# Kernel tuning notes

Measured on AMD Instinct MI355X. Metric: run time of the kernel, lower is better.

Reference implementation:

```python
import jax, jax.numpy as jnp
import numpy as np

K = 4  # kNN neighbors


def build_edges(density_maps, k):
    B, _, H, W = density_maps.shape
    N = H * W
    flat = density_maps.reshape(B, N)
    # [B, N, N] pairwise absolute density distance
    dist = jnp.abs(flat[:, :, None] - flat[:, None, :])
    # k nearest (excluding self at position 0)
    tgt = jnp.argsort(dist, axis=2)[:, :, 1:k + 1]  # [B, N, k]
    src = jnp.broadcast_to(jnp.arange(N)[None, :, None], (B, N, k))
    offset = (jnp.arange(B) * N)[:, None, None]
    src = (src + offset).reshape(-1)
    tgt = (tgt + offset).reshape(-1)
    n_total = B * N
    loops = jnp.arange(n_total)
    row = jnp.concatenate([src, loops])  # source nodes
    col = jnp.concatenate([tgt, loops])  # target nodes
    return row, col, n_total


def gcn_conv(x, row, col, W, b, n_nodes):
    # symmetric deg^-1/2 normalization, deg computed on target (col)
    deg = jax.ops.segment_sum(jnp.ones_like(col, dtype=x.dtype), col, num_segments=n_nodes)
    dinv = jnp.where(deg > 0, jax.lax.rsqrt(deg), 0.0)
    norm = dinv[row] * dinv[col]  # [E]
    h = x @ W  # transform first, then propagate
    msg = norm[:, None] * h[row]
    out = jax.ops.segment_sum(msg, col, num_segments=n_nodes)
    return out + b


def setup_inputs() -> dict:
    key = jax.random.key(0)
    k1, k2, k3, k4, k5, k6 = jax.random.split(key, 6)
    B, Cin, Chid, Cout, H, W = 4, 256, 512, 256, 64, 64
    density_maps = jax.random.uniform(k1, (B, 1, H, W), dtype=jnp.float32)
    feature_maps = jax.random.normal(k2, (B, Cin, H, W), dtype=jnp.float32)
    W1 = jax.random.normal(k3, (Cin, Chid), dtype=jnp.float32) * (1.0 / np.sqrt(Cin))
    b1 = jnp.zeros((Chid,), dtype=jnp.float32)
    W2 = jax.random.normal(k4, (Chid, Cout), dtype=jnp.float32) * (1.0 / np.sqrt(Chid))
    b2 = jnp.zeros((Cout,), dtype=jnp.float32)
    return {"density_maps": density_maps, "feature_maps": feature_maps,
            "W1": W1, "b1": b1, "W2": W2, "b2": b2}


def reference(density_maps, feature_maps, W1, b1, W2, b2):
    B, Cin, H, Wd = feature_maps.shape
    row, col, n_total = build_edges(density_maps, K)
    # [B,C,H,W] -> [B*H*W, C] node features
    x = feature_maps.transpose(0, 2, 3, 1).reshape(-1, Cin)
    h = jax.nn.relu(gcn_conv(x, row, col, W1, b1, n_total))
    out = jax.nn.relu(gcn_conv(h, row, col, W2, b2, n_total))
    return out.reshape(B, H, Wd, -1).transpose(0, 3, 1, 2)
```

## Files before the change

kernel.cpp:

```cpp
#include <hip/hip_runtime.h>
#include <hip/hip_bf16.h>
#include <stdint.h>

#define N_NODES 16384
#define NPB     4096
#define NB      4
#define KNN     4
#define WIN     12
#define NBUK    4096

typedef short bf16x8 __attribute__((ext_vector_type(8)));
typedef float f32x4 __attribute__((ext_vector_type(4)));
typedef unsigned short u16x8 __attribute__((ext_vector_type(8)));

__device__ __forceinline__ unsigned short f2bf(float f) {
  unsigned u = __float_as_uint(f);
  unsigned r = (u + 0x7fff + ((u >> 16) & 1)) >> 16;
  return (unsigned short)r;
}
__device__ __forceinline__ float bf2f(unsigned short u) {
  return __uint_as_float(((unsigned)u) << 16);
}

__global__ __launch_bounds__(1024)
void bucket_kernel(const float* __restrict__ dm,
                   unsigned long long* __restrict__ skeys_g,
                   int* __restrict__ rank_g,
                   float* __restrict__ dinv_g,
                   unsigned* __restrict__ mask_g) {
  __shared__ int sHist[4096];
  __shared__ int sCur[4096];
  __shared__ unsigned long long sKeys[4096];
  __shared__ unsigned sMask[4096];
  int* part1 = (int*)sKeys;
  int* part2 = (int*)(sKeys + 512);
  const int t = threadIdx.x, b = blockIdx.x;
  const float* d = dm + b * NPB;

  unsigned long long kv[4]; int bk[4];
#pragma unroll
  for (int r = 0; r < 4; ++r) sHist[t + r * 1024] = 0;
  __syncthreads();
#pragma unroll
  for (int r = 0; r < 4; ++r) {
    int i = t + r * 1024;
    float v = d[i];
    kv[r] = (((unsigned long long)__float_as_uint(v)) << 32) | (unsigned)i;
    int k = (int)(v * (float)NBUK); if (k > NBUK - 1) k = NBUK - 1;
    bk[r] = k;
    atomicAdd(&sHist[k], 1);
  }
  __syncthreads();
  int c0 = sHist[4 * t + 0], c1 = sHist[4 * t + 1];
  int c2 = sHist[4 * t + 2], c3 = sHist[4 * t + 3];
  part1[t] = c0 + c1 + c2 + c3;
  __syncthreads();
  if (t < 64) {
    int s = 0;
#pragma unroll
    for (int k = 0; k < 16; ++k) s += part1[16 * t + k];
    part2[t] = s;
  }
  __syncthreads();
  if (t == 0) {
    int a = 0;
    for (int u = 0; u < 64; ++u) { int v = part2[u]; part2[u] = a; a += v; }
  }
  __syncthreads();
  int base = part2[t >> 4];
  for (int k = (t >> 4) * 16; k < t; ++k) base += part1[k];
  sHist[4 * t + 0] = base; sCur[4 * t + 0] = base; base += c0;
  sHist[4 * t + 1] = base; sCur[4 * t + 1] = base; base += c1;
  sHist[4 * t + 2] = base; sCur[4 * t + 2] = base; base += c2;
  sHist[4 * t + 3] = base; sCur[4 * t + 3] = base;
  __syncthreads();
#pragma unroll
  for (int r = 0; r < 4; ++r) {
    int slot = atomicAdd(&sCur[bk[r]], 1);
    sKeys[slot] = kv[r];
  }
  __syncthreads();
#pragma unroll
  for (int r = 0; r < 4; ++r) {
    int g = t + r * 1024;
    int s0 = sHist[g];
    int s1 = (g == NPB - 1) ? NPB : sHist[g + 1];
    for (int i = s0 + 1; i < s1; ++i) {
      unsigned long long x = sKeys[i];
      int j = i - 1;
      while (j >= s0 && sKeys[j] > x) { sKeys[j + 1] = sKeys[j]; --j; }
      sKeys[j + 1] = x;
    }
  }
  __syncthreads();
#pragma unroll
  for (int r = 0; r < 4; ++r) {
    int i = t + r * 1024;
    sHist[i] = 1;
    sMask[i] = 0;
  }
  __syncthreads();
#pragma unroll
  for (int r = 0; r < 4; ++r) {
    int p = t + r * 1024;
    unsigned long long kp = sKeys[p];
    float di = __uint_as_float((unsigned)(kp >> 32));
    int lo = p - WIN; if (lo < 0) lo = 0;
    int hi = p + WIN; if (hi > NPB - 1) hi = NPB - 1;
    unsigned long long k0 = ~0ull, k1 = ~0ull, k2 = ~0ull, k3 = ~0ull, k4 = ~0ull;
    for (int q = lo; q <= hi; ++q) {
      unsigned long long key = sKeys[q];
      float v = __uint_as_float((unsigned)(key >> 32));
      float dist = fabsf(di - v);
      unsigned long long dk = (((unsigned long long)__float_as_uint(dist)) << 24) |
                              ((key & 0xfffull) << 12) | (unsigned)q;
      if (dk < k4) {
        if (dk < k0)      { k4 = k3; k3 = k2; k2 = k1; k1 = k0; k0 = dk; }
        else if (dk < k1) { k4 = k3; k3 = k2; k2 = k1; k1 = dk; }
        else if (dk < k2) { k4 = k3; k3 = k2; k2 = dk; }
        else if (dk < k3) { k4 = k3; k3 = dk; }
        else              { k4 = dk; }
      }
    }
    int t0 = (int)(k1 & 0xfff), t1 = (int)(k2 & 0xfff);
    int t2 = (int)(k3 & 0xfff), t3 = (int)(k4 & 0xfff);
    atomicAdd(&sHist[t0], 1); atomicOr(&sMask[t0], 1u << (p - t0 + WIN));
    atomicAdd(&sHist[t1], 1); atomicOr(&sMask[t1], 1u << (p - t1 + WIN));
    atomicAdd(&sHist[t2], 1); atomicOr(&sMask[t2], 1u << (p - t2 + WIN));
    atomicAdd(&sHist[t3], 1); atomicOr(&sMask[t3], 1u << (p - t3 + WIN));
  }
  __syncthreads();
#pragma unroll
  for (int r = 0; r < 4; ++r) {
    int i = t + r * 1024;
    unsigned long long k = sKeys[i];
    skeys_g[b * NPB + i] = k;
    rank_g[b * NPB + (int)(k & 0xffffffffull)] = i;
    dinv_g[b * NPB + i] = rsqrtf((float)sHist[i]);
    mask_g[b * NPB + i] = sMask[i];
  }
}

__global__ void cvt_all_kernel(const float* __restrict__ fm, unsigned short* __restrict__ px0,
                               const float* __restrict__ W1, unsigned short* __restrict__ W1t,
                               const float* __restrict__ W2, unsigned short* __restrict__ W2t,
                               const int* __restrict__ rank) {
  __shared__ float tile[64][33];
  int z = blockIdx.z;
  const float* in; unsigned short* outbase; int Rin, Cin, r0, c0;
  bool perm = false;
  if (z < NB) {
    in = fm + (size_t)z * 256 * 4096; outbase = px0 + (size_t)z * NPB * 256;
    Rin = 256; Cin = 4096; perm = true;
    c0 = blockIdx.x * 32; r0 = blockIdx.y * 64;
  } else {
    int id = blockIdx.y * 128 + blockIdx.x;
    if (id < 64)       { in = W1; outbase = W1t; Rin = 256; Cin = 512; c0 = (id & 15) * 32; r0 = (id >> 4) * 64; }
    else if (id < 128) { id -= 64; in = W2; outbase = W2t; Rin = 512; Cin = 256; c0 = (id & 7) * 32; r0 = (id >> 3) * 64; }
    else return;
  }
  int tx = threadIdx.x & 31, ty = threadIdx.x >> 5;
  const float* ip = in + (size_t)(r0 + ty) * Cin + c0 + tx;
#pragma unroll
  for (int i = 0; i < 8; ++i) tile[ty + 8 * i][tx] = ip[(size_t)(8 * i) * Cin];
  __syncthreads();
  int orow = threadIdx.x >> 3;
  int oseg = (threadIdx.x & 7) * 8;
  int outrow = c0 + orow;
  if (perm) outrow = rank[(size_t)z * NPB + outrow];
  unsigned short* op = outbase + (size_t)outrow * Rin + r0 + oseg;
  u16x8 o;
#pragma unroll
  for (int k = 0; k < 8; ++k) o[k] = f2bf(tile[oseg + k][orow]);
  *(u16x8*)op = o;
}

__global__ void transpose_kernel(const float* __restrict__ in, float* __restrict__ out,
                                 int Rin, int Cin) {
  __shared__ float tile[32][33];
  int c0 = blockIdx.x * 32, r0 = blockIdx.y * 32, b = blockIdx.z;
  int tx = threadIdx.x & 31, ty = threadIdx.x >> 5;
  const float* ip = in + ((size_t)b * Rin + r0) * Cin + c0;
#pragma unroll
  for (int i = 0; i < 32; i += 8) tile[ty + i][tx] = ip[(size_t)(ty + i) * Cin + tx];
  __syncthreads();
  float* op = out + ((size_t)b * Cin + c0) * Rin + r0;
#pragma unroll
  for (int i = 0; i < 32; i += 8) op[(size_t)(ty + i) * Rin + tx] = tile[tx][ty + i];
}

__global__ void prop_kernel(const unsigned short* __restrict__ in,
                            unsigned short* __restrict__ out,
                            const unsigned* __restrict__ mask,
                            const float* __restrict__ dinv) {
  int i = blockIdx.x * 8 + (threadIdx.x >> 5);
  int l = threadIdx.x & 31;
  unsigned m = mask[i];
  float a[8] = {};
#pragma unroll
  for (int off = 0; off < 2 * WIN + 1; ++off) {
    int c = ((m >> off) & 1) + (off == WIN);
    if (c) {
      int q = i + off - WIN;
      float dj = (float)c * dinv[q];
      u16x8 u = *(const u16x8*)(in + (size_t)q * 256 + l * 8);
#pragma unroll
      for (int k = 0; k < 8; ++k) a[k] = fmaf(dj, bf2f(u[k]), a[k]);
    }
  }
  float di = dinv[i];
  u16x8 o;
#pragma unroll
  for (int k = 0; k < 8; ++k) o[k] = f2bf(a[k] * di);
  *(u16x8*)(out + (size_t)i * 256 + l * 8) = o;
}

__global__ void prop2_kernel(const unsigned short* __restrict__ in,
                             float* __restrict__ out,
                             const unsigned* __restrict__ mask,
                             const float* __restrict__ dinv,
                             const float* __restrict__ bias,
                             const unsigned long long* __restrict__ skeys) {
  int i = blockIdx.x * 8 + (threadIdx.x >> 5);
  int l = threadIdx.x & 31;
  unsigned m = mask[i];
  float a[8] = {};
#pragma unroll
  for (int off = 0; off < 2 * WIN + 1; ++off) {
    int c = ((m >> off) & 1) + (off == WIN);
    if (c) {
      int q = i + off - WIN;
      float dj = (float)c * dinv[q];
      u16x8 u = *(const u16x8*)(in + (size_t)q * 256 + l * 8);
#pragma unroll
      for (int k = 0; k < 8; ++k) a[k] = fmaf(dj, bf2f(u[k]), a[k]);
    }
  }
  float di = dinv[i];
  int node = (i & ~(NPB - 1)) + (int)(skeys[i] & 0xffffffffull);
  float4 o0, o1;
  o0.x = fmaxf(a[0] * di + bias[l * 8 + 0], 0.f);
  o0.y = fmaxf(a[1] * di + bias[l * 8 + 1], 0.f);
  o0.z = fmaxf(a[2] * di + bias[l * 8 + 2], 0.f);
  o0.w = fmaxf(a[3] * di + bias[l * 8 + 3], 0.f);
  o1.x = fmaxf(a[4] * di + bias[l * 8 + 4], 0.f);
  o1.y = fmaxf(a[5] * di + bias[l * 8 + 5], 0.f);
  o1.z = fmaxf(a[6] * di + bias[l * 8 + 6], 0.f);
  o1.w = fmaxf(a[7] * di + bias[l * 8 + 7], 0.f);
  *(float4*)(out + (size_t)node * 256 + l * 8) = o0;
  *(float4*)(out + (size_t)node * 256 + l * 8 + 4) = o1;
}

template <bool BIAS_RELU, bool OUT_BF16, int NI>
__global__ __launch_bounds__(256)
void gemm_bf16_kernel(const unsigned short* __restrict__ A,
                      const unsigned short* __restrict__ Bt,
                      void* __restrict__ C, const float* __restrict__ bias,
                      int M, int N, int K) {
  __shared__ char lds[8192 + NI * 8192];
  const int tid = threadIdx.x;
  const int l = tid & 63, w = tid >> 6;
  const int bm = blockIdx.x * 64, bn = blockIdx.y * (64 * NI);
  f32x4 acc[4][NI] = {};

  for (int k0 = 0; k0 < K; k0 += 64) {
    __syncthreads();
#pragma unroll
    for (int q = 0; q < 2; ++q) {
      int o = q * 4096 + tid * 16;
      int r = o >> 7;
      int gc = ((o >> 4) & 7) ^ (r & 7);
      const char* srcA = (const char*)A + ((size_t)(bm + r) * K + k0) * 2 + gc * 16;
      __builtin_amdgcn_global_load_lds(
          (const __attribute__((address_space(1))) void*)srcA,
          (__attribute__((address_space(3))) void*)(lds + o), 16, 0, 0);
    }
#pragma unroll
    for (int q = 0; q < 2 * NI; ++q) {
      int o = q * 4096 + tid * 16;
      int r = o >> 7;
      int gc = ((o >> 4) & 7) ^ (r & 7);
      const char* srcB = (const char*)Bt + ((size_t)(bn + r) * K + k0) * 2 + gc * 16;
      __builtin_amdgcn_global_load_lds(
          (const __attribute__((address_space(1))) void*)srcB,
          (__attribute__((address_space(3))) void*)(lds + 8192 + o), 16, 0, 0);
    }
    __syncthreads();

#pragma unroll
    for (int kk = 0; kk < 64; kk += 32) {
      bf16x8 af[4], bf[NI];
      int gc = (kk >> 3) + (l >> 4);
#pragma unroll
      for (int mi = 0; mi < 4; ++mi) {
        int r = mi * 16 + (l & 15);
        af[mi] = *(const bf16x8*)(lds + r * 128 + ((gc ^ (r & 7)) << 4));
      }
#pragma unroll
      for (int ni = 0; ni < NI; ++ni) {
        int r = w * (16 * NI) + ni * 16 + (l & 15);
        bf[ni] = *(const bf16x8*)(lds + 8192 + r * 128 + ((gc ^ (r & 7)) << 4));
      }
#pragma unroll
      for (int mi = 0; mi < 4; ++mi)
#pragma unroll
        for (int ni = 0; ni < NI; ++ni)
          acc[mi][ni] = __builtin_amdgcn_mfma_f32_16x16x32_bf16(af[mi], bf[ni],
                                                                acc[mi][ni], 0, 0, 0);
    }
  }

#pragma unroll
  for (int mi = 0; mi < 4; ++mi) {
#pragma unroll
    for (int ni = 0; ni < NI; ++ni) {
      int row0 = bm + mi * 16 + ((l >> 4) << 2);
      int col = bn + w * (16 * NI) + ni * 16 + (l & 15);
      float bv = BIAS_RELU ? bias[col] : 0.f;
      f32x4 v = acc[mi][ni];
#pragma unroll
      for (int r = 0; r < 4; ++r) {
        float val = v[r];
        if (BIAS_RELU) val = fmaxf(val + bv, 0.f);
        if (OUT_BF16)
          ((unsigned short*)C)[(size_t)(row0 + r) * N + col] = f2bf(val);
        else
          ((float*)C)[(size_t)(row0 + r) * N + col] = val;
      }
    }
  }
}

extern "C" void kernel_launch(void* const* d_in, const int* in_sizes, int n_in,
                              void* d_out, int out_size, void* d_ws, size_t ws_size,
                              hipStream_t stream) {
  const float* dm = (const float*)d_in[0];
  const float* fm = (const float*)d_in[1];
  const float* W1 = (const float*)d_in[2];
  const float* b1 = (const float*)d_in[3];
  const float* W2 = (const float*)d_in[4];
  const float* b2 = (const float*)d_in[5];
  float* out = (float*)d_out;

  char* ws = (char*)d_ws;
  float*              dinv  = (float*)(ws + 0x050000);
  unsigned*           mask  = (unsigned*)(ws + 0x060000);
  unsigned long long* skeys = (unsigned long long*)(ws + 0x100000);
  int*                rank  = (int*)(ws + 0x130000);
  unsigned short*     W1t   = (unsigned short*)(ws + 0x190000);
  unsigned short*     W2t   = (unsigned short*)(ws + 0x1D0000);
  unsigned short*     px0   = (unsigned short*)(ws + 0x0400000);
  unsigned short*     px    = (unsigned short*)(ws + 0x0C00000);
  unsigned short*     h1    = (unsigned short*)(ws + 0x1400000);
  unsigned short*     t2    = (unsigned short*)(ws + 0x2400000);
  float*              xout  = (float*)(ws + 0x2C00000);
  (void)ws_size; (void)in_sizes; (void)n_in; (void)out_size;

  bucket_kernel<<<NB, 1024, 0, stream>>>(dm, skeys, rank, dinv, mask);

  cvt_all_kernel<<<dim3(128, 4, NB + 1), 256, 0, stream>>>(fm, px0, W1, W1t, W2, W2t, rank);

  prop_kernel<<<N_NODES / 8, 256, 0, stream>>>(px0, px, mask, dinv);
  gemm_bf16_kernel<true, true, 1><<<dim3(256, 8), 256, 0, stream>>>(
      px, W1t, h1, b1, 16384, 512, 256);

  gemm_bf16_kernel<false, true, 1><<<dim3(256, 4), 256, 0, stream>>>(
      h1, W2t, t2, nullptr, 16384, 256, 512);
  prop2_kernel<<<N_NODES / 8, 256, 0, stream>>>(t2, xout, mask, dinv, b2, skeys);

  transpose_kernel<<<dim3(8, 128, NB), 256, 0, stream>>>(xout, out, 4096, 256);
}
```

Baseline: 82.17 us.

## Stage neighbor-row halo tiles in LDS for both propagation kernels

```diff
diff --git a/kernel.cpp b/kernel.cpp
--- a/kernel.cpp
+++ b/kernel.cpp
@@ -8,6 +8,8 @@
 #define KNN     4
 #define WIN     12
 #define NBUK    4096
+#define PTILE   32
+#define HALO    (PTILE + 2 * WIN)
 
 typedef short bf16x8 __attribute__((ext_vector_type(8)));
 typedef float f32x4 __attribute__((ext_vector_type(4)));
@@ -189,66 +191,113 @@
   for (int i = 0; i < 32; i += 8) op[(size_t)(ty + i) * Rin + tx] = tile[tx][ty + i];
 }
 
-__global__ void prop_kernel(const unsigned short* __restrict__ in,
-                            unsigned short* __restrict__ out,
-                            const unsigned* __restrict__ mask,
-                            const float* __restrict__ dinv) {
-  int i = blockIdx.x * 8 + (threadIdx.x >> 5);
-  int l = threadIdx.x & 31;
-  unsigned m = mask[i];
-  float a[8] = {};
-#pragma unroll
-  for (int off = 0; off < 2 * WIN + 1; ++off) {
-    int c = ((m >> off) & 1) + (off == WIN);
-    if (c) {
-      int q = i + off - WIN;
-      float dj = (float)c * dinv[q];
-      u16x8 u = *(const u16x8*)(in + (size_t)q * 256 + l * 8);
-#pragma unroll
-      for (int k = 0; k < 8; ++k) a[k] = fmaf(dj, bf2f(u[k]), a[k]);
-    }
-  }
-  float di = dinv[i];
-  u16x8 o;
-#pragma unroll
-  for (int k = 0; k < 8; ++k) o[k] = f2bf(a[k] * di);
-  *(u16x8*)(out + (size_t)i * 256 + l * 8) = o;
-}
-
-__global__ void prop2_kernel(const unsigned short* __restrict__ in,
-                             float* __restrict__ out,
-                             const unsigned* __restrict__ mask,
-                             const float* __restrict__ dinv,
-                             const float* __restrict__ bias,
-                             const unsigned long long* __restrict__ skeys) {
-  int i = blockIdx.x * 8 + (threadIdx.x >> 5);
-  int l = threadIdx.x & 31;
-  unsigned m = mask[i];
-  float a[8] = {};
-#pragma unroll
-  for (int off = 0; off < 2 * WIN + 1; ++off) {
-    int c = ((m >> off) & 1) + (off == WIN);
-    if (c) {
-      int q = i + off - WIN;
-      float dj = (float)c * dinv[q];
-      u16x8 u = *(const u16x8*)(in + (size_t)q * 256 + l * 8);
-#pragma unroll
-      for (int k = 0; k < 8; ++k) a[k] = fmaf(dj, bf2f(u[k]), a[k]);
-    }
-  }
-  float di = dinv[i];
-  int node = (i & ~(NPB - 1)) + (int)(skeys[i] & 0xffffffffull);
-  float4 o0, o1;
-  o0.x = fmaxf(a[0] * di + bias[l * 8 + 0], 0.f);
-  o0.y = fmaxf(a[1] * di + bias[l * 8 + 1], 0.f);
-  o0.z = fmaxf(a[2] * di + bias[l * 8 + 2], 0.f);
-  o0.w = fmaxf(a[3] * di + bias[l * 8 + 3], 0.f);
-  o1.x = fmaxf(a[4] * di + bias[l * 8 + 4], 0.f);
-  o1.y = fmaxf(a[5] * di + bias[l * 8 + 5], 0.f);
-  o1.z = fmaxf(a[6] * di + bias[l * 8 + 6], 0.f);
-  o1.w = fmaxf(a[7] * di + bias[l * 8 + 7], 0.f);
-  *(float4*)(out + (size_t)node * 256 + l * 8) = o0;
-  *(float4*)(out + (size_t)node * 256 + l * 8 + 4) = o1;
+__global__ __launch_bounds__(256)
+void prop_kernel(const unsigned short* __restrict__ in,
+                 unsigned short* __restrict__ out,
+                 const unsigned* __restrict__ mask,
+                 const float* __restrict__ dinv) {
+  __shared__ char sRows[HALO * 512];
+  __shared__ float sDinv[HALO];
+  const int tid = threadIdx.x;
+  const int base = blockIdx.x * PTILE;
+  const long gbase = ((long)base - WIN) * 512;
+#pragma unroll
+  for (int k = 0; k < 7; ++k) {
+    int c = tid + k * 256;
+    long g = gbase + (long)c * 16;
+    if (g >= 0 && g < (long)N_NODES * 512)
+      __builtin_amdgcn_global_load_lds(
+          (const __attribute__((address_space(1))) void*)((const char*)in + g),
+          (__attribute__((address_space(3))) void*)(sRows + c * 16), 16, 0, 0);
+  }
+  if (tid < HALO) {
+    int q = base - WIN + tid;
+    sDinv[tid] = (q >= 0 && q < N_NODES) ? dinv[q] : 1.f;
+  }
+  __syncthreads();
+  const int hw = tid >> 5, l = tid & 31;
+  for (int s = 0; s < PTILE / 8; ++s) {
+    int i = base + hw * (PTILE / 8) + s;
+    unsigned m = mask[i];
+    float a[8] = {};
+#pragma unroll
+    for (int off = 0; off < 2 * WIN + 1; ++off) {
+      int c = ((m >> off) & 1) + (off == WIN);
+      if (c) {
+        int r = (i - base) + off;
+        float dj = (float)c * sDinv[r];
+        u16x8 u = *(const u16x8*)(sRows + r * 512 + l * 16);
+#pragma unroll
+        for (int k = 0; k < 8; ++k) a[k] = fmaf(dj, bf2f(u[k]), a[k]);
+      }
+    }
+    float di = sDinv[(i - base) + WIN];
+    u16x8 o;
+#pragma unroll
+    for (int k = 0; k < 8; ++k) o[k] = f2bf(a[k] * di);
+    *(u16x8*)(out + (size_t)i * 256 + l * 8) = o;
+  }
+}
+
+__global__ __launch_bounds__(256)
+void prop2_kernel(const unsigned short* __restrict__ in,
+                  float* __restrict__ out,
+                  const unsigned* __restrict__ mask,
+                  const float* __restrict__ dinv,
+                  const float* __restrict__ bias,
+                  const unsigned long long* __restrict__ skeys) {
+  __shared__ char sRows[HALO * 512];
+  __shared__ float sDinv[HALO];
+  const int tid = threadIdx.x;
+  const int base = blockIdx.x * PTILE;
+  const long gbase = ((long)base - WIN) * 512;
+#pragma unroll
+  for (int k = 0; k < 7; ++k) {
+    int c = tid + k * 256;
+    long g = gbase + (long)c * 16;
+    if (g >= 0 && g < (long)N_NODES * 512)
+      __builtin_amdgcn_global_load_lds(
+          (const __attribute__((address_space(1))) void*)((const char*)in + g),
+          (__attribute__((address_space(3))) void*)(sRows + c * 16), 16, 0, 0);
+  }
+  if (tid < HALO) {
+    int q = base - WIN + tid;
+    sDinv[tid] = (q >= 0 && q < N_NODES) ? dinv[q] : 1.f;
+  }
+  __syncthreads();
+  const int hw = tid >> 5, l = tid & 31;
+  float bv[8];
+#pragma unroll
+  for (int k = 0; k < 8; ++k) bv[k] = bias[l * 8 + k];
+  for (int s = 0; s < PTILE / 8; ++s) {
+    int i = base + hw * (PTILE / 8) + s;
+    unsigned m = mask[i];
+    float a[8] = {};
+#pragma unroll
+    for (int off = 0; off < 2 * WIN + 1; ++off) {
+      int c = ((m >> off) & 1) + (off == WIN);
+      if (c) {
+        int r = (i - base) + off;
+        float dj = (float)c * sDinv[r];
+        u16x8 u = *(const u16x8*)(sRows + r * 512 + l * 16);
+#pragma unroll
+        for (int k = 0; k < 8; ++k) a[k] = fmaf(dj, bf2f(u[k]), a[k]);
+      }
+    }
+    float di = sDinv[(i - base) + WIN];
+    int node = (i & ~(NPB - 1)) + (int)(skeys[i] & 0xffffffffull);
+    float4 o0, o1;
+    o0.x = fmaxf(a[0] * di + bv[0], 0.f);
+    o0.y = fmaxf(a[1] * di + bv[1], 0.f);
+    o0.z = fmaxf(a[2] * di + bv[2], 0.f);
+    o0.w = fmaxf(a[3] * di + bv[3], 0.f);
+    o1.x = fmaxf(a[4] * di + bv[4], 0.f);
+    o1.y = fmaxf(a[5] * di + bv[5], 0.f);
+    o1.z = fmaxf(a[6] * di + bv[6], 0.f);
+    o1.w = fmaxf(a[7] * di + bv[7], 0.f);
+    *(float4*)(out + (size_t)node * 256 + l * 8) = o0;
+    *(float4*)(out + (size_t)node * 256 + l * 8 + 4) = o1;
+  }
 }
 
 template <bool BIAS_RELU, bool OUT_BF16, int NI>
@@ -360,13 +409,13 @@
 
   cvt_all_kernel<<<dim3(128, 4, NB + 1), 256, 0, stream>>>(fm, px0, W1, W1t, W2, W2t, rank);
 
-  prop_kernel<<<N_NODES / 8, 256, 0, stream>>>(px0, px, mask, dinv);
+  prop_kernel<<<N_NODES / PTILE, 256, 0, stream>>>(px0, px, mask, dinv);
   gemm_bf16_kernel<true, true, 1><<<dim3(256, 8), 256, 0, stream>>>(
       px, W1t, h1, b1, 16384, 512, 256);
 
   gemm_bf16_kernel<false, true, 1><<<dim3(256, 4), 256, 0, stream>>>(
       h1, W2t, t2, nullptr, 16384, 256, 512);
-  prop2_kernel<<<N_NODES / 8, 256, 0, stream>>>(t2, xout, mask, dinv, b2, skeys);
+  prop2_kernel<<<N_NODES / PTILE, 256, 0, stream>>>(t2, xout, mask, dinv, b2, skeys);
 
   transpose_kernel<<<dim3(8, 128, NB), 256, 0, stream>>>(xout, out, 4096, 256);
 }
```

Result: slower. 86.61 us (+5.4%).
